# Performance work log

Hardware: AMD Instinct MI355X
Metric: run time of the kernel (lower is better)

## Reference

```python
import jax, jax.numpy as jnp
import numpy as np

D_HEAD = 64

def setup_inputs() -> dict:
    key = jax.random.key(0)
    ks = jax.random.split(key, 5)
    B, N, d_feat, d = 8, 2048, 256, 3
    f = jax.random.normal(ks[0], (B, N, d_feat), dtype=jnp.float32)
    x_tilde = jax.random.normal(ks[1], (B, N, d), dtype=jnp.float32)
    log_eps = jax.random.normal(ks[2], (B,), dtype=jnp.float32)
    W_q = jax.random.normal(ks[3], (d_feat + 1, D_HEAD), dtype=jnp.float32) * (1.0 / np.sqrt(d_feat + 1))
    W_k = jax.random.normal(ks[4], (d_feat + 1, D_HEAD), dtype=jnp.float32) * (1.0 / np.sqrt(d_feat + 1))
    return {"f": f, "x_tilde": x_tilde, "log_eps": log_eps, "W_q": W_q, "W_k": W_k}

def reference(f, x_tilde, log_eps, W_q, W_k):
    B, N, _ = f.shape
    # concat per-cloud log_eps scalar to every particle's features
    le = jnp.broadcast_to(log_eps[:, None, None], (B, N, 1)).astype(f.dtype)
    fc = jnp.concatenate([f, le], axis=-1)            # (B, N, d_feat+1)
    q = jnp.einsum('bnf,fh->bnh', fc, W_q)            # (B, N, d_head)
    k = jnp.einsum('bnf,fh->bnh', fc, W_k)            # (B, N, d_head)
    scale = jnp.asarray(np.sqrt(float(D_HEAD)), dtype=f.dtype)
    logits = jnp.einsum('bnh,bmh->bnm', q, k) / scale  # (B, N, N)
    N_f = jnp.asarray(N, dtype=f.dtype)
    col_softmax = jax.nn.softmax(logits, axis=1)       # softmax over QUERY axis
    pi = col_softmax / N_f                             # (B, N, N)
    # y_tilde = N * pi^T @ x_tilde
    y_tilde = N_f * jnp.einsum('bnm,bnd->bmd', pi, x_tilde)  # (B, N, d)
    return y_tilde, pi
```

## Files before the change

### kernel.cpp

```cpp
#include <hip/hip_runtime.h>
#include <hip/hip_bf16.h>

#define BB 8
#define NN 2048
#define DF 256
#define HH 64

using bf16x8 = __attribute__((ext_vector_type(8))) short;
using f32x4  = __attribute__((ext_vector_type(4))) float;
typedef unsigned short u16;

static __device__ __forceinline__ short bf_hi_bits(float v, float* hi_f) {
    __hip_bfloat16 h = __float2bfloat16(v);
    *hi_f = __bfloat162float(h);
    return __builtin_bit_cast(short, h);
}

__global__ __launch_bounds__(64) void wprep_kernel(
    const float* __restrict__ Wq, const float* __restrict__ Wk,
    u16* __restrict__ Wsp)
{
    const int fid  = blockIdx.x;
    const int kc   = fid >> 3, ct = fid & 7;
    const int lane = threadIdx.x;
    const float* W = (ct < 4) ? Wq : Wk;
    const int col  = (ct & 3) * 16 + (lane & 15);
    const int krow = kc * 32 + (lane >> 4) * 8;
    bf16x8 hv, lv;
#pragma unroll
    for (int j = 0; j < 8; ++j) {
        float w = W[(size_t)(krow + j) * HH + col];
        float hf, d;
        hv[j] = bf_hi_bits(w, &hf);
        lv[j] = bf_hi_bits(w - hf, &d);
    }
    u16* dst = Wsp + (size_t)fid * 1024 + lane * 8;
    *(bf16x8*)dst         = hv;
    *(bf16x8*)(dst + 512) = lv;
}

__global__ __launch_bounds__(256) void qk_mfma_kernel(
    const float* __restrict__ f, const float* __restrict__ log_eps,
    const float* __restrict__ Wq, const float* __restrict__ Wk,
    const u16* __restrict__ Wsp,
    __hip_bfloat16* __restrict__ Qs, __hip_bfloat16* __restrict__ Ks)
{
    __shared__ __align__(16) u16 wbuf[2][8192];

    const int tid  = threadIdx.x;
    const int wave = tid >> 6;
    const int lane = tid & 63;
    const int l15  = lane & 15, quad = lane >> 4;
    const int row0 = blockIdx.x * 64 + wave * 16;
    const int b    = (blockIdx.x * 64) >> 11;

    f32x4 acc[8] = {};
    const float* frow = f + (size_t)(row0 + l15) * DF + quad * 8;

    {
        const uint4* src = (const uint4*)(Wsp + tid * 32);
        uint4* dst = (uint4*)&wbuf[0][tid * 32];
#pragma unroll
        for (int i = 0; i < 4; ++i) dst[i] = src[i];
    }
    float4 a0 = *(const float4*)(frow);
    float4 a1 = *(const float4*)(frow + 4);
    __syncthreads();

    for (int kc = 0; kc < 8; ++kc) {
        const int cur = kc & 1;
        uint4 w0, w1, w2, w3;
        float4 na0, na1;
        if (kc < 7) {
            const uint4* src =
                (const uint4*)(Wsp + (size_t)(kc + 1) * 8192 + tid * 32);
            w0 = src[0]; w1 = src[1]; w2 = src[2]; w3 = src[3];
            na0 = *(const float4*)(frow + (kc + 1) * 32);
            na1 = *(const float4*)(frow + (kc + 1) * 32 + 4);
        }
        bf16x8 ah, al;
#pragma unroll
        for (int e = 0; e < 4; ++e) {
            float hf, d;
            float v0 = (&a0.x)[e], v1 = (&a1.x)[e];
            ah[e]     = bf_hi_bits(v0, &hf);
            al[e]     = bf_hi_bits(v0 - hf, &d);
            ah[e + 4] = bf_hi_bits(v1, &hf);
            al[e + 4] = bf_hi_bits(v1 - hf, &d);
        }
#pragma unroll
        for (int ct = 0; ct < 8; ++ct) {
            bf16x8 bh = *(const bf16x8*)&wbuf[cur][ct * 1024 + lane * 8];
            bf16x8 bl = *(const bf16x8*)&wbuf[cur][ct * 1024 + 512 + lane * 8];
            acc[ct] = __builtin_amdgcn_mfma_f32_16x16x32_bf16(ah, bh, acc[ct], 0, 0, 0);
            acc[ct] = __builtin_amdgcn_mfma_f32_16x16x32_bf16(ah, bl, acc[ct], 0, 0, 0);
            acc[ct] = __builtin_amdgcn_mfma_f32_16x16x32_bf16(al, bh, acc[ct], 0, 0, 0);
        }
        if (kc < 7) {
            uint4* dst = (uint4*)&wbuf[cur ^ 1][tid * 32];
            dst[0] = w0; dst[1] = w1; dst[2] = w2; dst[3] = w3;
            a0 = na0; a1 = na1;
        }
        __syncthreads();
    }

    const float le = log_eps[b];
#pragma unroll
    for (int ct = 0; ct < 8; ++ct) {
        const int h = (ct & 3) * 16 + l15;
        const float wlast = (ct < 4 ? Wq : Wk)[DF * HH + h];
        __hip_bfloat16* out = (ct < 4) ? Qs : Ks;
        const float sc = (ct < 4) ? 0.125f : 1.0f;
#pragma unroll
        for (int r = 0; r < 4; ++r) {
            int bn = row0 + quad * 4 + r;
            float v = (acc[ct][r] + le * wlast) * sc;
            __hip_bfloat16 hi = __float2bfloat16(v);
            __hip_bfloat16 lo = __float2bfloat16(v - __bfloat162float(hi));
            out[(size_t)bn * 128 + h]      = hi;
            out[(size_t)bn * 128 + 64 + h] = lo;
        }
    }
}

__global__ __launch_bounds__(512, 2) void attn_kernel(
    const u16* __restrict__ Qs, const u16* __restrict__ Ks,
    const float* __restrict__ x, float* __restrict__ y, float* __restrict__ pi)
{
    __shared__ float xs[NN * 3];
    __shared__ float cred[64];
    __shared__ float yred[8 * 4 * 16 * 3];

    const int tid   = threadIdx.x;
    const int strip = blockIdx.x;
    const int b     = blockIdx.y;
    const int m0    = strip * 64;
    const int wave  = tid >> 6;
    const int lane  = tid & 63;
    const int l15   = lane & 15;
    const int quad  = lane >> 4;

    if (tid < 64) cred[tid] = 0.f;
    for (int i = tid; i < NN * 3; i += 512) xs[i] = x[(size_t)b * NN * 3 + i];
    __syncthreads();

    bf16x8 bh[4][2], bl[4][2];
    {
        const u16* Kb = Ks + ((size_t)b * NN + m0) * 128;
#pragma unroll
        for (int ct = 0; ct < 4; ++ct) {
            const u16* kr = Kb + (size_t)(ct * 16 + l15) * 128;
#pragma unroll
            for (int ks = 0; ks < 2; ++ks) {
                int k0 = ks * 32 + quad * 8;
                bh[ct][ks] = *(const bf16x8*)(kr + k0);
                bl[ct][ks] = *(const bf16x8*)(kr + 64 + k0);
            }
        }
    }

    const u16* Qb = Qs + (size_t)b * NN * 128;
    float cs[4] = {0.f, 0.f, 0.f, 0.f};
    float yacc[4][3] = {};

    for (int rt = 0; rt < 8; ++rt) {
#pragma unroll
        for (int sr = 0; sr < 2; ++sr) {
            const int row0 = rt * 256 + wave * 32 + sr * 16;
            const u16* qr = Qb + (size_t)(row0 + l15) * 128;
            bf16x8 ah[2], al[2];
#pragma unroll
            for (int ks = 0; ks < 2; ++ks) {
                int k0 = ks * 32 + quad * 8;
                ah[ks] = *(const bf16x8*)(qr + k0);
                al[ks] = *(const bf16x8*)(qr + 64 + k0);
            }
            float xv[4][3];
#pragma unroll
            for (int r = 0; r < 4; ++r) {
                int row = row0 + quad * 4 + r;
                xv[r][0] = xs[row * 3 + 0];
                xv[r][1] = xs[row * 3 + 1];
                xv[r][2] = xs[row * 3 + 2];
            }
#pragma unroll
            for (int ct = 0; ct < 4; ++ct) {
                f32x4 acc = {0.f, 0.f, 0.f, 0.f};
#pragma unroll
                for (int ks = 0; ks < 2; ++ks) {
                    acc = __builtin_amdgcn_mfma_f32_16x16x32_bf16(ah[ks], bh[ct][ks], acc, 0, 0, 0);
                    acc = __builtin_amdgcn_mfma_f32_16x16x32_bf16(ah[ks], bl[ct][ks], acc, 0, 0, 0);
                    acc = __builtin_amdgcn_mfma_f32_16x16x32_bf16(al[ks], bh[ct][ks], acc, 0, 0, 0);
                }
                float s = 0.f;
#pragma unroll
                for (int r = 0; r < 4; ++r) {
                    float v = __expf(acc[r]);
                    s += v;
                    yacc[ct][0] = fmaf(v, xv[r][0], yacc[ct][0]);
                    yacc[ct][1] = fmaf(v, xv[r][1], yacc[ct][1]);
                    yacc[ct][2] = fmaf(v, xv[r][2], yacc[ct][2]);
                }
                cs[ct] += s;
            }
        }
    }

#pragma unroll
    for (int ct = 0; ct < 4; ++ct) {
        cs[ct] += __shfl_xor(cs[ct], 16);
        cs[ct] += __shfl_xor(cs[ct], 32);
#pragma unroll
        for (int d = 0; d < 3; ++d) {
            yacc[ct][d] += __shfl_xor(yacc[ct][d], 16);
            yacc[ct][d] += __shfl_xor(yacc[ct][d], 32);
        }
    }
    if (quad == 0) {
#pragma unroll
        for (int ct = 0; ct < 4; ++ct) {
            atomicAdd(&cred[ct * 16 + l15], cs[ct]);
#pragma unroll
            for (int d = 0; d < 3; ++d)
                yred[((wave * 4 + ct) * 16 + l15) * 3 + d] = yacc[ct][d];
        }
    }
    __syncthreads();

    if (tid < 192) {
        int c = tid / 3, d = tid - c * 3;
        int ct = c >> 4, cl = c & 15;
        float s = 0.f;
#pragma unroll
        for (int w = 0; w < 8; ++w)
            s += yred[((w * 4 + ct) * 16 + cl) * 3 + d];
        y[((size_t)b * NN + m0 + c) * 3 + d] = s / cred[c];
    }

    const float invN = 1.0f / (float)NN;
    float iv[4];
#pragma unroll
    for (int ct = 0; ct < 4; ++ct) iv[ct] = invN / cred[ct * 16 + l15];
    float* pib = pi + (size_t)b * NN * NN + m0;

    for (int rt = 0; rt < 8; ++rt) {
#pragma unroll
        for (int sr = 0; sr < 2; ++sr) {
            const int row0 = rt * 256 + wave * 32 + sr * 16;
            const u16* qr = Qb + (size_t)(row0 + l15) * 128;
            bf16x8 ah[2], al[2];
#pragma unroll
            for (int ks = 0; ks < 2; ++ks) {
                int k0 = ks * 32 + quad * 8;
                ah[ks] = *(const bf16x8*)(qr + k0);
                al[ks] = *(const bf16x8*)(qr + 64 + k0);
            }
#pragma unroll
            for (int ct = 0; ct < 4; ++ct) {
                f32x4 acc = {0.f, 0.f, 0.f, 0.f};
#pragma unroll
                for (int ks = 0; ks < 2; ++ks) {
                    acc = __builtin_amdgcn_mfma_f32_16x16x32_bf16(ah[ks], bh[ct][ks], acc, 0, 0, 0);
                    acc = __builtin_amdgcn_mfma_f32_16x16x32_bf16(ah[ks], bl[ct][ks], acc, 0, 0, 0);
                    acc = __builtin_amdgcn_mfma_f32_16x16x32_bf16(al[ks], bh[ct][ks], acc, 0, 0, 0);
                }
                float* op = pib + (size_t)(row0 + quad * 4) * NN + ct * 16 + l15;
#pragma unroll
                for (int r = 0; r < 4; ++r)
                    op[(size_t)r * NN] = __expf(acc[r]) * iv[ct];
            }
        }
    }
}

extern "C" void kernel_launch(void* const* d_in, const int* in_sizes, int n_in,
                              void* d_out, int out_size, void* d_ws, size_t ws_size,
                              hipStream_t stream) {
    const float* f  = (const float*)d_in[0];
    const float* x  = (const float*)d_in[1];
    const float* le = (const float*)d_in[2];
    const float* Wq = (const float*)d_in[3];
    const float* Wk = (const float*)d_in[4];

    float* y  = (float*)d_out;
    float* pi = (float*)d_out + (size_t)BB * NN * 3;

    __hip_bfloat16* Qs = (__hip_bfloat16*)d_ws;
    __hip_bfloat16* Ks = Qs + (size_t)BB * NN * 128;
    u16* Wsp = (u16*)pi;

    wprep_kernel<<<dim3(64), 64, 0, stream>>>(Wq, Wk, Wsp);
    qk_mfma_kernel<<<dim3(BB * NN / 64), 256, 0, stream>>>(f, le, Wq, Wk, Wsp, Qs, Ks);
    attn_kernel<<<dim3(32, BB), 512, 0, stream>>>((const u16*)Qs, (const u16*)Ks,
                                                  x, y, pi);
}
```

Baseline: 194.3 us.

## Split attention into column-sum and pi-write kernels for more parallelism

Replaces the single attention kernel (256 blocks, each doing both the column-sum pass and the pi-write pass) with separate kernels. A colsum kernel writes column sums and y, with sums staged in the pi buffer. A 1024-block pi kernel recomputes logits and writes pi. A small cleanup kernel then fixes the first rows of pi that overlapped the csbuf scratch. This raises grid parallelism for the bandwidth-bound pi write and adds register double-buffering of Q fragments. The cost is an extra launch and an awkward aliasing/cleanup path that depends on exact buffer overlap.

```diff
diff --git a/kernel.cpp b/kernel.cpp
--- a/kernel.cpp
+++ b/kernel.cpp
@@ -14,6 +14,11 @@
     __hip_bfloat16 h = __float2bfloat16(v);
     *hi_f = __bfloat162float(h);
     return __builtin_bit_cast(short, h);
+}
+
+static __device__ __forceinline__ float bfbits2f(u16 v) {
+    unsigned int x = ((unsigned int)v) << 16;
+    return __builtin_bit_cast(float, x);
 }
 
 __global__ __launch_bounds__(64) void wprep_kernel(
@@ -123,153 +128,204 @@
     }
 }
 
-__global__ __launch_bounds__(512, 2) void attn_kernel(
+#define LOADQF(AH, AL, ROW0)                                                   \
+    {                                                                          \
+        const u16* qr = Qb + (size_t)((ROW0) + l15) * 128;                     \
+        _Pragma("unroll")                                                      \
+        for (int ks = 0; ks < 2; ++ks) {                                       \
+            int k0 = ks * 32 + quad * 8;                                       \
+            AH[ks] = *(const bf16x8*)(qr + k0);                                \
+            AL[ks] = *(const bf16x8*)(qr + 64 + k0);                           \
+        }                                                                      \
+    }
+
+__global__ __launch_bounds__(256) void colsum_kernel(
     const u16* __restrict__ Qs, const u16* __restrict__ Ks,
-    const float* __restrict__ x, float* __restrict__ y, float* __restrict__ pi)
+    const float* __restrict__ x, float* __restrict__ y,
+    float* __restrict__ csbuf)
 {
     __shared__ float xs[NN * 3];
-    __shared__ float cred[64];
-    __shared__ float yred[8 * 4 * 16 * 3];
 
     const int tid   = threadIdx.x;
-    const int strip = blockIdx.x;
-    const int b     = blockIdx.y;
+    const int bid   = blockIdx.x;
+    const int b     = bid & 7;
+    const int strip = bid >> 3;
     const int m0    = strip * 64;
     const int wave  = tid >> 6;
     const int lane  = tid & 63;
     const int l15   = lane & 15;
     const int quad  = lane >> 4;
 
-    if (tid < 64) cred[tid] = 0.f;
-    for (int i = tid; i < NN * 3; i += 512) xs[i] = x[(size_t)b * NN * 3 + i];
+    for (int i = tid; i < NN * 3; i += 256) xs[i] = x[(size_t)b * NN * 3 + i];
     __syncthreads();
 
-    bf16x8 bh[4][2], bl[4][2];
+    bf16x8 bh[2], bl[2];
     {
-        const u16* Kb = Ks + ((size_t)b * NN + m0) * 128;
-#pragma unroll
-        for (int ct = 0; ct < 4; ++ct) {
-            const u16* kr = Kb + (size_t)(ct * 16 + l15) * 128;
-#pragma unroll
-            for (int ks = 0; ks < 2; ++ks) {
-                int k0 = ks * 32 + quad * 8;
-                bh[ct][ks] = *(const bf16x8*)(kr + k0);
-                bl[ct][ks] = *(const bf16x8*)(kr + 64 + k0);
-            }
+        const u16* kr = Ks + ((size_t)b * NN + m0 + wave * 16 + l15) * 128;
+#pragma unroll
+        for (int ks = 0; ks < 2; ++ks) {
+            int k0 = ks * 32 + quad * 8;
+            bh[ks] = *(const bf16x8*)(kr + k0);
+            bl[ks] = *(const bf16x8*)(kr + 64 + k0);
         }
     }
 
     const u16* Qb = Qs + (size_t)b * NN * 128;
-    float cs[4] = {0.f, 0.f, 0.f, 0.f};
-    float yacc[4][3] = {};
-
-    for (int rt = 0; rt < 8; ++rt) {
-#pragma unroll
-        for (int sr = 0; sr < 2; ++sr) {
-            const int row0 = rt * 256 + wave * 32 + sr * 16;
-            const u16* qr = Qb + (size_t)(row0 + l15) * 128;
-            bf16x8 ah[2], al[2];
-#pragma unroll
-            for (int ks = 0; ks < 2; ++ks) {
-                int k0 = ks * 32 + quad * 8;
-                ah[ks] = *(const bf16x8*)(qr + k0);
-                al[ks] = *(const bf16x8*)(qr + 64 + k0);
-            }
-            float xv[4][3];
-#pragma unroll
-            for (int r = 0; r < 4; ++r) {
-                int row = row0 + quad * 4 + r;
-                xv[r][0] = xs[row * 3 + 0];
-                xv[r][1] = xs[row * 3 + 1];
-                xv[r][2] = xs[row * 3 + 2];
-            }
-#pragma unroll
-            for (int ct = 0; ct < 4; ++ct) {
-                f32x4 acc = {0.f, 0.f, 0.f, 0.f};
-#pragma unroll
-                for (int ks = 0; ks < 2; ++ks) {
-                    acc = __builtin_amdgcn_mfma_f32_16x16x32_bf16(ah[ks], bh[ct][ks], acc, 0, 0, 0);
-                    acc = __builtin_amdgcn_mfma_f32_16x16x32_bf16(ah[ks], bl[ct][ks], acc, 0, 0, 0);
-                    acc = __builtin_amdgcn_mfma_f32_16x16x32_bf16(al[ks], bh[ct][ks], acc, 0, 0, 0);
-                }
-                float s = 0.f;
-#pragma unroll
-                for (int r = 0; r < 4; ++r) {
-                    float v = __expf(acc[r]);
-                    s += v;
-                    yacc[ct][0] = fmaf(v, xv[r][0], yacc[ct][0]);
-                    yacc[ct][1] = fmaf(v, xv[r][1], yacc[ct][1]);
-                    yacc[ct][2] = fmaf(v, xv[r][2], yacc[ct][2]);
-                }
-                cs[ct] += s;
-            }
-        }
-    }
-
-#pragma unroll
-    for (int ct = 0; ct < 4; ++ct) {
-        cs[ct] += __shfl_xor(cs[ct], 16);
-        cs[ct] += __shfl_xor(cs[ct], 32);
-#pragma unroll
-        for (int d = 0; d < 3; ++d) {
-            yacc[ct][d] += __shfl_xor(yacc[ct][d], 16);
-            yacc[ct][d] += __shfl_xor(yacc[ct][d], 32);
-        }
-    }
+    float cs = 0.f, yac0 = 0.f, yac1 = 0.f, yac2 = 0.f;
+
+#define CSBODY(ROW0, AH, AL)                                                   \
+    {                                                                          \
+        f32x4 acc = {0.f, 0.f, 0.f, 0.f};                                      \
+        _Pragma("unroll")                                                      \
+        for (int ks = 0; ks < 2; ++ks) {                                       \
+            acc = __builtin_amdgcn_mfma_f32_16x16x32_bf16(AH[ks], bh[ks], acc, 0, 0, 0); \
+            acc = __builtin_amdgcn_mfma_f32_16x16x32_bf16(AH[ks], bl[ks], acc, 0, 0, 0); \
+            acc = __builtin_amdgcn_mfma_f32_16x16x32_bf16(AL[ks], bh[ks], acc, 0, 0, 0); \
+        }                                                                      \
+        _Pragma("unroll")                                                      \
+        for (int r = 0; r < 4; ++r) {                                          \
+            float v = __expf(acc[r]);                                          \
+            int row = (ROW0) + quad * 4 + r;                                   \
+            cs += v;                                                           \
+            yac0 = fmaf(v, xs[row * 3 + 0], yac0);                             \
+            yac1 = fmaf(v, xs[row * 3 + 1], yac1);                             \
+            yac2 = fmaf(v, xs[row * 3 + 2], yac2);                             \
+        }                                                                      \
+    }
+
+    {
+        bf16x8 ahA[2], alA[2], ahB[2], alB[2];
+        LOADQF(ahA, alA, 0);
+        for (int it = 0; it < 128; it += 2) {
+            LOADQF(ahB, alB, (it + 1) * 16);
+            CSBODY(it * 16, ahA, alA);
+            if (it + 2 < 128) LOADQF(ahA, alA, (it + 2) * 16);
+            CSBODY((it + 1) * 16, ahB, alB);
+        }
+    }
+#undef CSBODY
+
+    cs   += __shfl_xor(cs, 16);   cs   += __shfl_xor(cs, 32);
+    yac0 += __shfl_xor(yac0, 16); yac0 += __shfl_xor(yac0, 32);
+    yac1 += __shfl_xor(yac1, 16); yac1 += __shfl_xor(yac1, 32);
+    yac2 += __shfl_xor(yac2, 16); yac2 += __shfl_xor(yac2, 32);
+
     if (quad == 0) {
-#pragma unroll
-        for (int ct = 0; ct < 4; ++ct) {
-            atomicAdd(&cred[ct * 16 + l15], cs[ct]);
-#pragma unroll
-            for (int d = 0; d < 3; ++d)
-                yred[((wave * 4 + ct) * 16 + l15) * 3 + d] = yacc[ct][d];
-        }
-    }
+        const int col = m0 + wave * 16 + l15;
+        csbuf[(size_t)b * NN + col] = cs;
+        float inv = 1.0f / cs;
+        float* yp = y + ((size_t)b * NN + col) * 3;
+        yp[0] = yac0 * inv;
+        yp[1] = yac1 * inv;
+        yp[2] = yac2 * inv;
+    }
+}
+
+__global__ __launch_bounds__(256, 4) void pi_kernel(
+    const u16* __restrict__ Qs, const u16* __restrict__ Ks,
+    const float* __restrict__ csbuf, float* __restrict__ pi)
+{
+    const int tid   = threadIdx.x;
+    const int bid   = blockIdx.x;
+    const int b     = bid & 7;
+    const int t     = bid >> 3;
+    const int rc    = t & 7;
+    const int strip = t >> 3;
+    const int m0    = strip * 128;
+    const int wave  = tid >> 6;
+    const int lane  = tid & 63;
+    const int l15   = lane & 15;
+    const int quad  = lane >> 4;
+
+    const int c0 = m0 + wave * 32 + l15;
+    const int c1 = c0 + 16;
+    const float invN = 1.0f / (float)NN;
+    const float iv0 = invN / csbuf[(size_t)b * NN + c0];
+    const float iv1 = invN / csbuf[(size_t)b * NN + c1];
+
+    bf16x8 bh[2][2], bl[2][2];
+#pragma unroll
+    for (int ct = 0; ct < 2; ++ct) {
+        const u16* kr = Ks + ((size_t)b * NN + m0 + wave * 32 + ct * 16 + l15) * 128;
+#pragma unroll
+        for (int ks = 0; ks < 2; ++ks) {
+            int k0 = ks * 32 + quad * 8;
+            bh[ct][ks] = *(const bf16x8*)(kr + k0);
+            bl[ct][ks] = *(const bf16x8*)(kr + 64 + k0);
+        }
+    }
+
+    const u16* Qb = Qs + (size_t)b * NN * 128;
+    const int row_base = rc * 256;
+    const bool guard0 = (b == 0) && (rc == 0);
+
+#define PIBODY(IT, AH, AL)                                                     \
+    {                                                                          \
+        const int row0 = row_base + (IT) * 16;                                 \
+        const bool full = !(guard0 && (IT) == 0);                              \
+        _Pragma("unroll")                                                      \
+        for (int ct = 0; ct < 2; ++ct) {                                       \
+            f32x4 acc = {0.f, 0.f, 0.f, 0.f};                                  \
+            _Pragma("unroll")                                                  \
+            for (int ks = 0; ks < 2; ++ks) {                                   \
+                acc = __builtin_amdgcn_mfma_f32_16x16x32_bf16(AH[ks], bh[ct][ks], acc, 0, 0, 0); \
+                acc = __builtin_amdgcn_mfma_f32_16x16x32_bf16(AH[ks], bl[ct][ks], acc, 0, 0, 0); \
+                acc = __builtin_amdgcn_mfma_f32_16x16x32_bf16(AL[ks], bh[ct][ks], acc, 0, 0, 0); \
+            }                                                                  \
+            const float iv = (ct == 0) ? iv0 : iv1;                            \
+            const int cc   = (ct == 0) ? c0 : c1;                              \
+            float* op = pi + ((size_t)b * NN + row0 + quad * 4) * NN + cc;     \
+            if (full || quad >= 2) {                                           \
+                _Pragma("unroll")                                              \
+                for (int r = 0; r < 4; ++r)                                    \
+                    op[(size_t)r * NN] = __expf(acc[r]) * iv;                  \
+            }                                                                  \
+        }                                                                      \
+    }
+
+    {
+        bf16x8 ahA[2], alA[2], ahB[2], alB[2];
+        LOADQF(ahA, alA, row_base);
+        for (int it = 0; it < 16; it += 2) {
+            LOADQF(ahB, alB, row_base + (it + 1) * 16);
+            PIBODY(it, ahA, alA);
+            if (it + 2 < 16) LOADQF(ahA, alA, row_base + (it + 2) * 16);
+            PIBODY(it + 1, ahB, alB);
+        }
+    }
+#undef PIBODY
+}
+
+__global__ __launch_bounds__(512) void cleanup_kernel(
+    const u16* __restrict__ Qs, const u16* __restrict__ Ks,
+    float* __restrict__ pi)
+{
+    __shared__ float csl[256];
+    __shared__ u16 ql[8 * 128];
+
+    const int s   = blockIdx.x;
+    const int tid = threadIdx.x;
+
+    if (tid < 256) csl[tid] = pi[s * 256 + tid];
+    for (int i = tid; i < 1024; i += 512) ql[i] = Qs[i];
     __syncthreads();
 
-    if (tid < 192) {
-        int c = tid / 3, d = tid - c * 3;
-        int ct = c >> 4, cl = c & 15;
-        float s = 0.f;
-#pragma unroll
-        for (int w = 0; w < 8; ++w)
-            s += yred[((w * 4 + ct) * 16 + cl) * 3 + d];
-        y[((size_t)b * NN + m0 + c) * 3 + d] = s / cred[c];
-    }
-
     const float invN = 1.0f / (float)NN;
-    float iv[4];
-#pragma unroll
-    for (int ct = 0; ct < 4; ++ct) iv[ct] = invN / cred[ct * 16 + l15];
-    float* pib = pi + (size_t)b * NN * NN + m0;
-
-    for (int rt = 0; rt < 8; ++rt) {
-#pragma unroll
-        for (int sr = 0; sr < 2; ++sr) {
-            const int row0 = rt * 256 + wave * 32 + sr * 16;
-            const u16* qr = Qb + (size_t)(row0 + l15) * 128;
-            bf16x8 ah[2], al[2];
-#pragma unroll
-            for (int ks = 0; ks < 2; ++ks) {
-                int k0 = ks * 32 + quad * 8;
-                ah[ks] = *(const bf16x8*)(qr + k0);
-                al[ks] = *(const bf16x8*)(qr + 64 + k0);
-            }
-#pragma unroll
-            for (int ct = 0; ct < 4; ++ct) {
-                f32x4 acc = {0.f, 0.f, 0.f, 0.f};
-#pragma unroll
-                for (int ks = 0; ks < 2; ++ks) {
-                    acc = __builtin_amdgcn_mfma_f32_16x16x32_bf16(ah[ks], bh[ct][ks], acc, 0, 0, 0);
-                    acc = __builtin_amdgcn_mfma_f32_16x16x32_bf16(ah[ks], bl[ct][ks], acc, 0, 0, 0);
-                    acc = __builtin_amdgcn_mfma_f32_16x16x32_bf16(al[ks], bh[ct][ks], acc, 0, 0, 0);
-                }
-                float* op = pib + (size_t)(row0 + quad * 4) * NN + ct * 16 + l15;
-#pragma unroll
-                for (int r = 0; r < 4; ++r)
-                    op[(size_t)r * NN] = __expf(acc[r]) * iv[ct];
-            }
-        }
+#pragma unroll
+    for (int k = 0; k < 4; ++k) {
+        const int idx = tid + k * 512;
+        const int row = idx >> 8;
+        const int cl  = idx & 255;
+        const int col = s * 256 + cl;
+        const u16* kk = Ks + (size_t)col * 128;
+        float dot = 0.f;
+#pragma unroll 8
+        for (int h = 0; h < 64; ++h) {
+            float qf = bfbits2f(ql[row * 128 + h]) + bfbits2f(ql[row * 128 + 64 + h]);
+            float kf = bfbits2f(kk[h]) + bfbits2f(kk[64 + h]);
+            dot = fmaf(qf, kf, dot);
+        }
+        pi[(size_t)row * NN + col] = __expf(dot) * invN / csl[cl];
     }
 }
 
@@ -287,10 +343,14 @@
 
     __hip_bfloat16* Qs = (__hip_bfloat16*)d_ws;
     __hip_bfloat16* Ks = Qs + (size_t)BB * NN * 128;
-    u16* Wsp = (u16*)pi;
+    u16*   Wsp   = (u16*)pi;
+    float* csbuf = pi;
 
     wprep_kernel<<<dim3(64), 64, 0, stream>>>(Wq, Wk, Wsp);
     qk_mfma_kernel<<<dim3(BB * NN / 64), 256, 0, stream>>>(f, le, Wq, Wk, Wsp, Qs, Ks);
-    attn_kernel<<<dim3(32, BB), 512, 0, stream>>>((const u16*)Qs, (const u16*)Ks,
-                                                  x, y, pi);
-}
+    colsum_kernel<<<dim3(256), 256, 0, stream>>>((const u16*)Qs, (const u16*)Ks,
+                                                 x, y, csbuf);
+    pi_kernel<<<dim3(1024), 256, 0, stream>>>((const u16*)Qs, (const u16*)Ks,
+                                              csbuf, pi);
+    cleanup_kernel<<<dim3(8), 512, 0, stream>>>((const u16*)Qs, (const u16*)Ks, pi);
+}
```

Measured after the change: 260.2 us. 33.9% more time.
